# Optimization experiments

Measured on AMD Instinct MI355X. Metric: run time of the kernel, lower is better.

Reference implementation:

```python
import jax, jax.numpy as jnp
import numpy as np

B = 8388608  # 2^23 rows -> each [B,4] activation is 128 MB
N_LAYERS = 99


def setup_inputs() -> dict:
    key = jax.random.key(0)
    ks = jax.random.split(key, 7)
    return {
        "x": jax.random.normal(ks[0], (B, 2), dtype=jnp.float32),
        "W_in": jax.random.normal(ks[1], (2, 4), dtype=jnp.float32) * 0.5,
        "b_in": jax.random.normal(ks[2], (4,), dtype=jnp.float32) * 0.1,
        "Ws": jax.random.normal(ks[3], (N_LAYERS, 4, 4), dtype=jnp.float32) * 0.5,
        "bs": jax.random.normal(ks[4], (N_LAYERS, 4), dtype=jnp.float32) * 0.1,
        "W_out": jax.random.normal(ks[5], (4, 1), dtype=jnp.float32) * 0.5,
        "b_out": jax.random.normal(ks[6], (1,), dtype=jnp.float32) * 0.1,
    }


def reference(x, W_in, b_in, Ws, bs, W_out, b_out):
    # input layer + relu
    out = jax.nn.relu(x @ W_in + b_in)  # [B, 4]
    skip = out
    # torch condition `if i % 5 and i != 0` == residual whenever i % 5 != 0
    flags = (jnp.arange(N_LAYERS) % 5) != 0  # [99] bool

    def step(carry, layer):
        out, skip = carry
        W, b, flag = layer  # W: [4,4], b: [4]
        h = jax.nn.relu(out @ W + b)  # Linear(4,4) + ReLU
        new_out = jnp.where(flag, h + skip, h)
        new_skip = jnp.where(flag, new_out, skip)
        return (new_out, new_skip), None

    (out, skip), _ = jax.lax.scan(step, (out, skip), (Ws, bs, flags))
    return out @ W_out + b_out  # [B, 1]
```

## Files before the change

kernel.cpp:

```cpp
#include <hip/hip_runtime.h>


#define NLAYERS 99

__global__ __launch_bounds__(256) void skipmlp_kernel(
    const float* __restrict__ x,
    const float* __restrict__ W_in,
    const float* __restrict__ b_in,
    const float* __restrict__ Ws,
    const float* __restrict__ bs,
    const float* __restrict__ W_out,
    const float* __restrict__ b_out,
    float* __restrict__ out,
    int B)
{
    __shared__ float4 lw[NLAYERS * 5];

    const float4* __restrict__ Ws4 = reinterpret_cast<const float4*>(Ws);
    const float4* __restrict__ bs4 = reinterpret_cast<const float4*>(bs);
    for (int j4 = threadIdx.x; j4 < NLAYERS * 5; j4 += 256) {
        int layer = j4 / 5;
        int q = j4 - layer * 5;
        lw[j4] = (q < 4) ? Ws4[layer * 4 + q] : bs4[layer];
    }
    __syncthreads();

    int row = blockIdx.x * blockDim.x + threadIdx.x;
    if (row >= B) return;

    const float2 xv = *reinterpret_cast<const float2*>(x + (size_t)row * 2u);

    float o0 = fmaxf(fmaf(xv.x, W_in[0], fmaf(xv.y, W_in[4], b_in[0])), 0.f);
    float o1 = fmaxf(fmaf(xv.x, W_in[1], fmaf(xv.y, W_in[5], b_in[1])), 0.f);
    float o2 = fmaxf(fmaf(xv.x, W_in[2], fmaf(xv.y, W_in[6], b_in[2])), 0.f);
    float o3 = fmaxf(fmaf(xv.x, W_in[3], fmaf(xv.y, W_in[7], b_in[3])), 0.f);

    float s0 = o0, s1 = o1, s2 = o2, s3 = o3;

    float4 c0 = lw[0], c1 = lw[1], c2 = lw[2], c3 = lw[3], cb = lw[4];

#define STEP(RES, NEXT) {                                                     \
        float4 n0 = lw[(NEXT)*5+0], n1 = lw[(NEXT)*5+1], n2 = lw[(NEXT)*5+2], \
               n3 = lw[(NEXT)*5+3], nb = lw[(NEXT)*5+4];                      \
        float i0, i1, i2, i3;                                                 \
        if (RES) { i0 = cb.x + s0; i1 = cb.y + s1; i2 = cb.z + s2; i3 = cb.w + s3; } \
        else     { i0 = cb.x;      i1 = cb.y;      i2 = cb.z;      i3 = cb.w; }      \
        float p0 = fmaf(o0, c0.x, fmaf(o1, c1.x, fmaf(o2, c2.x, fmaf(o3, c3.x, i0)))); \
        float p1 = fmaf(o0, c0.y, fmaf(o1, c1.y, fmaf(o2, c2.y, fmaf(o3, c3.y, i1)))); \
        float p2 = fmaf(o0, c0.z, fmaf(o1, c1.z, fmaf(o2, c2.z, fmaf(o3, c3.z, i2)))); \
        float p3 = fmaf(o0, c0.w, fmaf(o1, c1.w, fmaf(o2, c2.w, fmaf(o3, c3.w, i3)))); \
        if (RES) {                                                            \
            o0 = fmaxf(p0, s0); o1 = fmaxf(p1, s1);                           \
            o2 = fmaxf(p2, s2); o3 = fmaxf(p3, s3);                           \
            s0 = o0; s1 = o1; s2 = o2; s3 = o3;                               \
        } else {                                                              \
            o0 = fmaxf(p0, 0.f); o1 = fmaxf(p1, 0.f);                         \
            o2 = fmaxf(p2, 0.f); o3 = fmaxf(p3, 0.f);                         \
        }                                                                     \
        c0 = n0; c1 = n1; c2 = n2; c3 = n3; cb = nb;                          \
    }

    for (int base = 0; base < 95; base += 5) {
        STEP(false, base + 1);
        STEP(true,  base + 2);
        STEP(true,  base + 3);
        STEP(true,  base + 4);
        STEP(true,  base + 5);
    }
    STEP(false, 96);
    STEP(true,  97);
    STEP(true,  98);
    STEP(true,  98);
#undef STEP

    float y = fmaf(o0, W_out[0], fmaf(o1, W_out[1], fmaf(o2, W_out[2], o3 * W_out[3]))) + b_out[0];
    out[row] = y;
}

extern "C" void kernel_launch(void* const* d_in, const int* in_sizes, int n_in,
                              void* d_out, int out_size, void* d_ws, size_t ws_size,
                              hipStream_t stream) {
    const float* x     = (const float*)d_in[0];
    const float* W_in  = (const float*)d_in[1];
    const float* b_in  = (const float*)d_in[2];
    const float* Ws    = (const float*)d_in[3];
    const float* bs    = (const float*)d_in[4];
    const float* W_out = (const float*)d_in[5];
    const float* b_out = (const float*)d_in[6];
    float* out = (float*)d_out;

    const int B = in_sizes[0] / 2;
    const int block = 256;
    const int grid = (B + block - 1) / block;

    skipmlp_kernel<<<grid, block, 0, stream>>>(x, W_in, b_in, Ws, bs, W_out, b_out, out, B);
}
```

Measured before the change: 539.4 us.

## Fold residual into weight diagonal and read weights as uniform scalar loads

A small prep kernel adds identity to the weight matrices of layers whose input equals the skip, so those layers use fmax(p, o) and drop the separate skip adds. The main kernel now keeps only biases in LDS and reads weights straight from global memory through wave-uniform pointers, which the compiler can turn into scalar loads instead of LDS reads. This cuts LDS traffic and some VALU adds, at the cost of an extra kernel launch and a workspace write. It also changes the FP rounding order slightly.

```diff
diff --git a/kernel.cpp b/kernel.cpp
--- a/kernel.cpp
+++ b/kernel.cpp
@@ -3,26 +3,34 @@
 
 #define NLAYERS 99
 
+__global__ void prep_kernel(const float* __restrict__ Ws,
+                            const float* __restrict__ bs,
+                            float* __restrict__ wmod) {
+    int i = blockIdx.x * blockDim.x + threadIdx.x;
+    if (i < NLAYERS * 16) {
+        int layer = i >> 4;
+        int e = i & 15;
+        float w = Ws[i];
+        if ((layer % 5) >= 2 && (e % 5) == 0) w += 1.0f;
+        wmod[i] = w;
+    }
+    if (i < NLAYERS * 4) wmod[NLAYERS * 16 + i] = bs[i];
+}
+
 __global__ __launch_bounds__(256) void skipmlp_kernel(
     const float* __restrict__ x,
     const float* __restrict__ W_in,
     const float* __restrict__ b_in,
-    const float* __restrict__ Ws,
-    const float* __restrict__ bs,
+    const float* __restrict__ wmod,
     const float* __restrict__ W_out,
     const float* __restrict__ b_out,
     float* __restrict__ out,
     int B)
 {
-    __shared__ float4 lw[NLAYERS * 5];
-
-    const float4* __restrict__ Ws4 = reinterpret_cast<const float4*>(Ws);
-    const float4* __restrict__ bs4 = reinterpret_cast<const float4*>(bs);
-    for (int j4 = threadIdx.x; j4 < NLAYERS * 5; j4 += 256) {
-        int layer = j4 / 5;
-        int q = j4 - layer * 5;
-        lw[j4] = (q < 4) ? Ws4[layer * 4 + q] : bs4[layer];
-    }
+    __shared__ float4 lb[NLAYERS];
+    if (threadIdx.x < NLAYERS)
+        lb[threadIdx.x] =
+            reinterpret_cast<const float4*>(wmod + NLAYERS * 16)[threadIdx.x];
     __syncthreads();
 
     int row = blockIdx.x * blockDim.x + threadIdx.x;
@@ -37,40 +45,45 @@
 
     float s0 = o0, s1 = o1, s2 = o2, s3 = o3;
 
-    float4 c0 = lw[0], c1 = lw[1], c2 = lw[2], c3 = lw[3], cb = lw[4];
+    float4 bc = lb[0];
 
-#define STEP(RES, NEXT) {                                                     \
-        float4 n0 = lw[(NEXT)*5+0], n1 = lw[(NEXT)*5+1], n2 = lw[(NEXT)*5+2], \
-               n3 = lw[(NEXT)*5+3], nb = lw[(NEXT)*5+4];                      \
+#define STEP(MODE, I, NEXT) {                                                 \
+        float4 bn = lb[NEXT];                                                 \
+        const float* __restrict__ W = wmod + (I) * 16;                        \
         float i0, i1, i2, i3;                                                 \
-        if (RES) { i0 = cb.x + s0; i1 = cb.y + s1; i2 = cb.z + s2; i3 = cb.w + s3; } \
-        else     { i0 = cb.x;      i1 = cb.y;      i2 = cb.z;      i3 = cb.w; }      \
-        float p0 = fmaf(o0, c0.x, fmaf(o1, c1.x, fmaf(o2, c2.x, fmaf(o3, c3.x, i0)))); \
-        float p1 = fmaf(o0, c0.y, fmaf(o1, c1.y, fmaf(o2, c2.y, fmaf(o3, c3.y, i1)))); \
-        float p2 = fmaf(o0, c0.z, fmaf(o1, c1.z, fmaf(o2, c2.z, fmaf(o3, c3.z, i2)))); \
-        float p3 = fmaf(o0, c0.w, fmaf(o1, c1.w, fmaf(o2, c2.w, fmaf(o3, c3.w, i3)))); \
-        if (RES) {                                                            \
+        if (MODE == 1) { i0 = bc.x + s0; i1 = bc.y + s1;                      \
+                         i2 = bc.z + s2; i3 = bc.w + s3; }                    \
+        else           { i0 = bc.x; i1 = bc.y; i2 = bc.z; i3 = bc.w; }        \
+        float p0 = fmaf(o0, W[ 0], fmaf(o1, W[ 4], fmaf(o2, W[ 8], fmaf(o3, W[12], i0)))); \
+        float p1 = fmaf(o0, W[ 1], fmaf(o1, W[ 5], fmaf(o2, W[ 9], fmaf(o3, W[13], i1)))); \
+        float p2 = fmaf(o0, W[ 2], fmaf(o1, W[ 6], fmaf(o2, W[10], fmaf(o3, W[14], i2)))); \
+        float p3 = fmaf(o0, W[ 3], fmaf(o1, W[ 7], fmaf(o2, W[11], fmaf(o3, W[15], i3)))); \
+        if (MODE == 0) {                                                      \
+            o0 = fmaxf(p0, 0.f); o1 = fmaxf(p1, 0.f);                         \
+            o2 = fmaxf(p2, 0.f); o3 = fmaxf(p3, 0.f);                         \
+        } else if (MODE == 1) {                                               \
             o0 = fmaxf(p0, s0); o1 = fmaxf(p1, s1);                           \
             o2 = fmaxf(p2, s2); o3 = fmaxf(p3, s3);                           \
             s0 = o0; s1 = o1; s2 = o2; s3 = o3;                               \
         } else {                                                              \
-            o0 = fmaxf(p0, 0.f); o1 = fmaxf(p1, 0.f);                         \
-            o2 = fmaxf(p2, 0.f); o3 = fmaxf(p3, 0.f);                         \
+            o0 = fmaxf(p0, o0); o1 = fmaxf(p1, o1);                           \
+            o2 = fmaxf(p2, o2); o3 = fmaxf(p3, o3);                           \
+            s0 = o0; s1 = o1; s2 = o2; s3 = o3;                               \
         }                                                                     \
-        c0 = n0; c1 = n1; c2 = n2; c3 = n3; cb = nb;                          \
+        bc = bn;                                                              \
     }
 
     for (int base = 0; base < 95; base += 5) {
-        STEP(false, base + 1);
-        STEP(true,  base + 2);
-        STEP(true,  base + 3);
-        STEP(true,  base + 4);
-        STEP(true,  base + 5);
+        STEP(0, base + 0, base + 1);
+        STEP(1, base + 1, base + 2);
+        STEP(2, base + 2, base + 3);
+        STEP(2, base + 3, base + 4);
+        STEP(2, base + 4, base + 5);
     }
-    STEP(false, 96);
-    STEP(true,  97);
-    STEP(true,  98);
-    STEP(true,  98);
+    STEP(0, 95, 96);
+    STEP(1, 96, 97);
+    STEP(2, 97, 98);
+    STEP(2, 98, 98);
 #undef STEP
 
     float y = fmaf(o0, W_out[0], fmaf(o1, W_out[1], fmaf(o2, W_out[2], o3 * W_out[3]))) + b_out[0];
@@ -88,10 +101,13 @@
     const float* W_out = (const float*)d_in[5];
     const float* b_out = (const float*)d_in[6];
     float* out = (float*)d_out;
+    float* wmod = (float*)d_ws;
 
     const int B = in_sizes[0] / 2;
+
+    prep_kernel<<<(NLAYERS * 16 + 255) / 256, 256, 0, stream>>>(Ws, bs, wmod);
+
     const int block = 256;
     const int grid = (B + block - 1) / block;
-
-    skipmlp_kernel<<<grid, block, 0, stream>>>(x, W_in, b_in, Ws, bs, W_out, b_out, out, B);
+    skipmlp_kernel<<<grid, block, 0, stream>>>(x, W_in, b_in, wmod, W_out, b_out, out, B);
 }
```

Measured after the change: 464.6 us. 1.16x faster.
